# Kernel optimization log

Hardware: AMD Instinct MI355X
Metric: run time of the kernel (lower is better)

Reference implementation:

```python
import math
import jax, jax.numpy as jnp
import numpy as np
from jax import lax

# FPN anchor layout: 1024x768 image, strides {4,8,16,32,64}, 3 anchors/location
NUM_PER_LEVEL = (147456, 36864, 9216, 2304, 576)
A_TOTAL = sum(NUM_PER_LEVEL)
BATCH = 8
PRE_NMS_TOP_N = 1000   # testing
POST_NMS_TOP_N = 1000  # testing
NMS_THRESH = 0.7
SCORE_THRESH = 0.0
MIN_SIZE = 1.0
IMG_H, IMG_W = 768.0, 1024.0
BBOX_XFORM_CLIP = math.log(1000.0 / 16.0)


def setup_inputs() -> dict:
    key = jax.random.key(0)
    k1, k2, k3, k4, k5, k6 = jax.random.split(key, 6)
    objectness = jax.random.normal(k1, (BATCH, A_TOTAL), jnp.float32)
    pred_bbox_deltas = jax.random.normal(k2, (BATCH, A_TOTAL, 4), jnp.float32) * 0.2
    # valid anchor boxes (x1, y1, x2, y2)
    cx = jax.random.uniform(k3, (A_TOTAL,), jnp.float32) * IMG_W
    cy = jax.random.uniform(k4, (A_TOTAL,), jnp.float32) * IMG_H
    w = 16.0 + jax.random.uniform(k5, (A_TOTAL,), jnp.float32) * 176.0
    h = 16.0 + jax.random.uniform(k6, (A_TOTAL,), jnp.float32) * 176.0
    anchors = jnp.stack([cx - 0.5 * w, cy - 0.5 * h, cx + 0.5 * w, cy + 0.5 * h], -1)
    return {"objectness": objectness, "pred_bbox_deltas": pred_bbox_deltas, "anchors": anchors}


def _nms_image(boxes, scores, lvl, valid):
    """batched_nms (level-offset trick) + post-NMS top-k, fixed shapes.
    boxes [K,4], scores [K], lvl [K] int, valid [K] bool -> [POST_NMS_TOP_N, 5]"""
    K = boxes.shape[0]
    s = jnp.where(valid, scores, -1.0)
    order = jnp.argsort(-s)  # decreasing score (invalid last)
    b = boxes[order]
    s = s[order]
    v = valid[order]
    # offset boxes per level so cross-level boxes never overlap (torchvision batched_nms)
    offset = lvl[order].astype(b.dtype) * (jnp.max(lax.stop_gradient(boxes)) + 1.0)
    nb = lax.stop_gradient(b) + offset[:, None]
    area = (nb[:, 2] - nb[:, 0]) * (nb[:, 3] - nb[:, 1])
    lt = jnp.maximum(nb[:, None, :2], nb[None, :, :2])  # [K,K,2]
    rb = jnp.minimum(nb[:, None, 2:], nb[None, :, 2:])
    wh = jnp.clip(rb - lt, 0.0)
    inter = wh[..., 0] * wh[..., 1]
    iou = inter / jnp.maximum(area[:, None] + area[None, :] - inter, 1e-9)
    pos = jnp.arange(K)

    def body(keep, i):
        sup = keep[i] & (iou[i] > NMS_THRESH) & (pos > i)
        return keep & ~sup, None

    keep, _ = lax.scan(body, v, pos)
    masked = jnp.where(keep, s, -1.0)
    top_s, top_i = lax.top_k(masked, POST_NMS_TOP_N)  # kept, decreasing score
    sel_b = b[top_i]
    ok = top_s > -0.5
    sel_b = jnp.where(ok[:, None], sel_b, 0.0)
    top_s = jnp.where(ok, top_s, 0.0)
    return jnp.concatenate([sel_b, top_s[:, None]], axis=-1)


def reference(objectness, pred_bbox_deltas, anchors):
    # --- box decode (BoxCoder, weights (1,1,1,1)) ---
    wa = anchors[:, 2] - anchors[:, 0]
    ha = anchors[:, 3] - anchors[:, 1]
    cxa = anchors[:, 0] + 0.5 * wa
    cya = anchors[:, 1] + 0.5 * ha
    dx, dy = pred_bbox_deltas[..., 0], pred_bbox_deltas[..., 1]
    dw = jnp.minimum(pred_bbox_deltas[..., 2], BBOX_XFORM_CLIP)
    dh = jnp.minimum(pred_bbox_deltas[..., 3], BBOX_XFORM_CLIP)
    pcx = dx * wa + cxa
    pcy = dy * ha + cya
    pw = jnp.exp(dw) * wa
    ph = jnp.exp(dh) * ha
    proposals = jnp.stack(
        [pcx - 0.5 * pw, pcy - 0.5 * ph, pcx + 0.5 * pw, pcy + 0.5 * ph], axis=-1
    )  # [B, A, 4]

    # --- per-level pre-NMS top-k (_get_top_n_idx) ---
    levels = jnp.concatenate(
        [jnp.full((n,), i, jnp.int32) for i, n in enumerate(NUM_PER_LEVEL)]
    )
    idx_parts = []
    off = 0
    for n in NUM_PER_LEVEL:
        k = min(PRE_NMS_TOP_N, n)
        _, ti = lax.top_k(objectness[:, off:off + n], k)
        idx_parts.append(ti + off)
        off += n
    top_idx = jnp.concatenate(idx_parts, axis=1)  # [B, K]

    scores = jax.nn.sigmoid(jnp.take_along_axis(objectness, top_idx, axis=1))
    lvl = levels[top_idx]
    boxes = jnp.take_along_axis(proposals, top_idx[..., None], axis=1)  # [B,K,4]

    # --- clip to image ---
    x1 = jnp.clip(boxes[..., 0], 0.0, IMG_W)
    y1 = jnp.clip(boxes[..., 1], 0.0, IMG_H)
    x2 = jnp.clip(boxes[..., 2], 0.0, IMG_W)
    y2 = jnp.clip(boxes[..., 3], 0.0, IMG_H)
    boxes = jnp.stack([x1, y1, x2, y2], axis=-1)

    # remove_small_boxes + score threshold (as validity mask; fixed shapes)
    valid = ((x2 - x1) >= MIN_SIZE) & ((y2 - y1) >= MIN_SIZE) & (scores >= SCORE_THRESH)

    # --- per-image batched NMS + post-NMS top-k ---
    return jax.vmap(_nms_image)(boxes, scores, lvl, valid)  # [B, POST_NMS_TOP_N, 5]
```

## Files before the change

kernel.cpp:

```cpp
#include <hip/hip_runtime.h>
#include <math.h>

#pragma clang fp contract(off)

#define A_TOTAL 196416
#define BATCH 8
#define KTOT 4576
#define NLEV 5
#define MSPLIT 16
#define RCAP 6144

static __device__ const int d_aoff[NLEV] = {0, 147456, 184320, 193536, 195840};
static __device__ const int d_n[NLEV]    = {147456, 36864, 9216, 2304, 576};
static __device__ const int d_k[NLEV]    = {1000, 1000, 1000, 1000, 576};
static __device__ const int d_spl[NLEV]  = {8, 2, 1, 1, 1};
static __device__ const int d_bp[NLEV]   = {0, 8, 10, 11, 12};
static __device__ const int d_pb_l[13]    = {0,0,0,0,0,0,0,0,1,1,2,3,4};
static __device__ const int d_pb_part[13] = {0,1,2,3,4,5,6,7,0,1,0,0,0};

#define TM_IOU (0.699999988079071044921875 + 0x1p-25)

__device__ inline unsigned int mono(float f) {
  unsigned int u = __float_as_uint(f);
  return (u & 0x80000000u) ? ~u : (u | 0x80000000u);
}
__device__ inline float imono(unsigned int m) {
  return __uint_as_float((m & 0x80000000u) ? (m & 0x7FFFFFFFu) : ~m);
}

__device__ inline int cnt_gt(const float* A, int n, float s) {
  int lo = 0, hi = n;
  while (lo < hi) { int mid = (lo + hi) >> 1; if (A[mid] > s) lo = mid + 1; else hi = mid; }
  return lo;
}
__device__ inline int cnt_ge(const float* A, int n, float s) {
  int lo = 0, hi = n;
  while (lo < hi) { int mid = (lo + hi) >> 1; if (A[mid] >= s) lo = mid + 1; else hi = mid; }
  return lo;
}

__global__ __launch_bounds__(1024) void k_hist(const float* __restrict__ obj,
                                               int* __restrict__ hist_g,
                                               int* __restrict__ cnt_g,
                                               float* __restrict__ maxblk,
                                               float* __restrict__ out) {
  int blk = blockIdx.x;
  int tid = threadIdx.x;
  if (blk == 0) {
    for (int i = tid; i < 40; i += 1024) { maxblk[i] = 0.0f; cnt_g[i] = 0; }
  }
  int b = blk / 13, pb = blk % 13;
  if (pb == 0) {
    float* ob = out + (size_t)b * 5000;
    for (int i = tid; i < 5000; i += 1024) ob[i] = 0.0f;
  }
  int l = d_pb_l[pb], part = d_pb_part[pb];
  int slice = d_n[l] / d_spl[l];
  int start = d_aoff[l] + part * slice;
  const float4* p4 = (const float4*)(obj + (size_t)b * A_TOTAL + start);
  int s4 = slice >> 2;
  __shared__ int h[4096];
  for (int i = tid; i < 4096; i += 1024) h[i] = 0;
  __syncthreads();
  for (int i = tid; i < s4; i += 1024) {
    float4 v = p4[i];
    atomicAdd(&h[mono(v.x) >> 20], 1);
    atomicAdd(&h[mono(v.y) >> 20], 1);
    atomicAdd(&h[mono(v.z) >> 20], 1);
    atomicAdd(&h[mono(v.w) >> 20], 1);
  }
  __syncthreads();
  int* outp = hist_g + (size_t)blk * 4096;
  for (int i = tid; i < 4096; i += 1024) outp[i] = h[i];
}

__global__ __launch_bounds__(1024) void k_collect(const float* __restrict__ obj,
                                                  const int* __restrict__ hist_g,
                                                  int* __restrict__ cnt_g,
                                                  unsigned long long* __restrict__ cand_g) {
  int blk = blockIdx.x;
  int b = blk / 13, pb = blk % 13;
  int l = d_pb_l[pb], part = d_pb_part[pb];
  int bl = b * NLEV + l;
  const int k = d_k[l];
  int tid = threadIdx.x, lane = tid & 63;
  __shared__ int t[4096];
  __shared__ int grp[256];
  __shared__ unsigned int sP;
  __shared__ __align__(16) unsigned long long lbuf[RCAP];
  __shared__ int s_cnt, s_base;
  int parts = d_spl[l];
  const int* hb = hist_g + (size_t)(b * 13 + d_bp[l]) * 4096;
  for (int bin = tid; bin < 4096; bin += 1024) {
    int s = 0;
    for (int p = 0; p < parts; ++p) s += hb[p * 4096 + bin];
    t[bin] = s;
  }
  if (tid == 0) s_cnt = 0;
  __syncthreads();
  if (tid < 256) {
    int s = 0;
    for (int j = 0; j < 16; ++j) s += t[tid * 16 + j];
    grp[tid] = s;
  }
  __syncthreads();
  if (tid < 64) {
    int g0 = grp[4 * tid], g1 = grp[4 * tid + 1];
    int g2 = grp[4 * tid + 2], g3 = grp[4 * tid + 3];
    int q = g0 + g1 + g2 + g3;
    int x = q;
#pragma unroll
    for (int off = 1; off < 64; off <<= 1) {
      int y = __shfl_down(x, off);
      if (tid + off < 64) x += y;
    }
    int Qn = x - q;
    int best = -1;
    if (x >= k) best = 4 * tid;
    if (g1 + g2 + g3 + Qn >= k) best = 4 * tid + 1;
    if (g2 + g3 + Qn >= k) best = 4 * tid + 2;
    if (g3 + Qn >= k) best = 4 * tid + 3;
#pragma unroll
    for (int off = 1; off < 64; off <<= 1) best = max(best, __shfl_xor(best, off));
    int gstar = best;
    int partl = 0;
    if (4 * tid > gstar) partl += g0;
    if (4 * tid + 1 > gstar) partl += g1;
    if (4 * tid + 2 > gstar) partl += g2;
    if (4 * tid + 3 > gstar) partl += g3;
#pragma unroll
    for (int off = 1; off < 64; off <<= 1) partl += __shfl_xor(partl, off);
    int cum = partl;
    int tb = (tid < 16) ? t[gstar * 16 + tid] : 0;
    int Tx = tb;
#pragma unroll
    for (int off = 1; off < 16; off <<= 1) {
      int y = __shfl_down(Tx, off);
      if (tid + off < 16) Tx += y;
    }
    int bestd = -1;
    if (tid < 16 && cum + Tx >= k) bestd = tid;
#pragma unroll
    for (int off = 1; off < 64; off <<= 1) bestd = max(bestd, __shfl_xor(bestd, off));
    if (tid == 0) sP = (unsigned int)(gstar * 16 + bestd);
  }
  __syncthreads();
  unsigned int P = sP;
  int slice = d_n[l] / parts;
  int start = d_aoff[l] + part * slice;
  const float4* p4 = (const float4*)(obj + (size_t)b * A_TOTAL + start);
  int s4 = slice >> 2;
  int lbase = part * slice;
  for (int i = tid; i < s4; i += 1024) {
    float4 v = p4[i];
    unsigned int a[4] = {mono(v.x), mono(v.y), mono(v.z), mono(v.w)};
    bool q0 = (a[0] >> 20) >= P, q1 = (a[1] >> 20) >= P;
    bool q2 = (a[2] >> 20) >= P, q3 = (a[3] >> 20) >= P;
    if (__ballot(q0 | q1 | q2 | q3)) {
      bool qs[4] = {q0, q1, q2, q3};
#pragma unroll
      for (int c = 0; c < 4; ++c) {
        unsigned long long mb = __ballot(qs[c]);
        if (mb) {
          int base;
          if (lane == 0) base = atomicAdd(&s_cnt, __popcll(mb));
          base = __shfl(base, 0);
          if (qs[c]) {
            int slot = base + __popcll(mb & ((1ull << lane) - 1ull));
            if (slot < RCAP) {
              int idx = lbase + 4 * i + c;
              lbuf[slot] = ((unsigned long long)a[c] << 32) |
                           (unsigned int)(~(unsigned int)idx);
            }
          }
        }
      }
    }
  }
  __syncthreads();
  int cnt = min(s_cnt, RCAP);
  if (tid == 0) s_base = atomicAdd(&cnt_g[bl], cnt);
  __syncthreads();
  int base = s_base;
  for (int i = tid; i < cnt; i += 1024) {
    int slot = base + i;
    if (slot < RCAP) cand_g[(size_t)bl * RCAP + slot] = lbuf[i];
  }
}

__device__ inline float decode_emit(unsigned long long e, int rank, int b,
                                    int k, int aoff, int bl,
                                    const float* __restrict__ deltas,
                                    const float* __restrict__ anchors,
                                    float* __restrict__ sc0,
                                    float4* __restrict__ box0) {
  if (rank >= k) return 0.0f;
  unsigned int k32 = (unsigned int)(e >> 32);
  unsigned int idx = ~(unsigned int)(e & 0xFFFFFFFFull);
  float o = imono(k32);
  int gidx = aoff + (int)idx;
  const float* dl = deltas + ((size_t)b * A_TOTAL + gidx) * 4;
  const float* an = anchors + (size_t)gidx * 4;
  float a0 = an[0], a1 = an[1], a2 = an[2], a3 = an[3];
  float wa = a2 - a0, ha = a3 - a1;
  float cxa = a0 + 0.5f * wa, cya = a1 + 0.5f * ha;
  float dx = dl[0], dy = dl[1];
  const float CLIPV = 4.135166556742356f;
  float dw = fminf(dl[2], CLIPV), dh = fminf(dl[3], CLIPV);
  float pcx = dx * wa + cxa;
  float pcy = dy * ha + cya;
  float pw = (float)exp((double)dw) * wa;
  float ph = (float)exp((double)dh) * ha;
  float x1 = pcx - 0.5f * pw, y1 = pcy - 0.5f * ph;
  float x2 = pcx + 0.5f * pw, y2 = pcy + 0.5f * ph;
  x1 = fminf(fmaxf(x1, 0.0f), 1024.0f);
  x2 = fminf(fmaxf(x2, 0.0f), 1024.0f);
  y1 = fminf(fmaxf(y1, 0.0f), 768.0f);
  y2 = fminf(fmaxf(y2, 0.0f), 768.0f);
  float s = (float)(1.0 / (1.0 + exp(-(double)o)));
  bool valid = ((x2 - x1) >= 1.0f) && ((y2 - y1) >= 1.0f) && (s >= 0.0f);
  sc0[bl * 1024 + rank] = valid ? s : -1.0f;
  box0[bl * 1024 + rank] = make_float4(x1, y1, x2, y2);
  return fmaxf(fmaxf(x1, y1), fmaxf(x2, y2));
}

__global__ __launch_bounds__(1024) void k_rankdec(const unsigned long long* __restrict__ cand_g,
                                                  const int* __restrict__ cnt_g,
                                                  const float* __restrict__ deltas,
                                                  const float* __restrict__ anchors,
                                                  float* __restrict__ sc0,
                                                  float4* __restrict__ box0,
                                                  float* __restrict__ maxblk) {
  int bl = blockIdx.x;
  int b = bl / NLEV, l = bl % NLEV;
  const int k = d_k[l], aoff = d_aoff[l];
  int cnt = min(cnt_g[bl], RCAP);
  int tid = threadIdx.x, lane = tid & 63, w = tid >> 6;
  __shared__ int h[4096], sfx[4096], offs[4096];
  __shared__ __align__(16) unsigned long long sorted[RCAP];
  __shared__ int s_wsum[16];
  __shared__ unsigned int s_max;
  if (tid == 0) s_max = 0u;
  for (int i = tid; i < 4096; i += 1024) h[i] = 0;
  __syncthreads();
  const unsigned long long* src = cand_g + (size_t)bl * RCAP;
  for (int i = tid; i < cnt; i += 1024)
    atomicAdd(&h[(unsigned int)(src[i] >> 52)], 1);
  __syncthreads();
  int t4 = tid * 4;
  int h0 = h[t4], h1 = h[t4 + 1], h2 = h[t4 + 2], h3 = h[t4 + 3];
  int mysum = h0 + h1 + h2 + h3;
  int x = mysum;
#pragma unroll
  for (int off = 1; off < 64; off <<= 1) {
    int y = __shfl_down(x, off);
    if (lane + off < 64) x += y;
  }
  if (lane == 0) s_wsum[w] = x;
  __syncthreads();
  int wsuf = 0;
  for (int ww = w + 1; ww < 16; ++ww) wsuf += s_wsum[ww];
  int excl = (x - mysum) + wsuf;
  sfx[t4 + 3] = excl;
  sfx[t4 + 2] = excl + h3;
  sfx[t4 + 1] = excl + h3 + h2;
  sfx[t4]     = excl + h3 + h2 + h1;
  offs[t4] = sfx[t4]; offs[t4 + 1] = sfx[t4 + 1];
  offs[t4 + 2] = sfx[t4 + 2]; offs[t4 + 3] = sfx[t4 + 3];
  __syncthreads();
  for (int i = tid; i < cnt; i += 1024) {
    unsigned long long e = src[i];
    int pos = atomicAdd(&offs[(unsigned int)(e >> 52)], 1);
    sorted[pos] = e;
  }
  __syncthreads();
  float mx = 0.0f;
  for (int p = tid; p < cnt; p += 1024) {
    unsigned long long e = sorted[p];
    unsigned int bin = (unsigned int)(e >> 52);
    int s0 = sfx[bin], s1 = s0 + h[bin];
    int rank = s0;
    for (int j = s0; j < s1; ++j) rank += (sorted[j] > e);
    if (rank < k)
      mx = fmaxf(mx, decode_emit(e, rank, b, k, aoff, bl, deltas, anchors, sc0, box0));
  }
#pragma unroll
  for (int s = 1; s < 64; s <<= 1) mx = fmaxf(mx, __shfl_xor(mx, s));
  if (lane == 0) atomicMax(&s_max, __float_as_uint(mx));
  __syncthreads();
  if (tid == 0) maxblk[bl] = __uint_as_float(s_max);
}

__global__ __launch_bounds__(1024) void k_mask(const float* __restrict__ sc0,
                                               const float4* __restrict__ box0,
                                               const float* __restrict__ maxblk,
                                               float* __restrict__ lvlsc,
                                               float4* __restrict__ lvlraw,
                                               int* __restrict__ g_V,
                                               unsigned long long* __restrict__ masks) {
  int blk = blockIdx.x;
  int bl = blk / MSPLIT, part = blk % MSPLIT;
  int b = bl / NLEV, l = bl % NLEV;
  const int k = d_k[l];
  int tid = threadIdx.x, lane = tid & 63, w = tid >> 6;
  __shared__ float4 lbox[1024];
  __shared__ float s_mv;
  __shared__ int s_wcnt[16];
  if (w == 0) {
    float v = (lane < NLEV) ? maxblk[b * NLEV + lane] : 0.0f;
#pragma unroll
    for (int s = 1; s < 64; s <<= 1) v = fmaxf(v, __shfl_xor(v, s));
    if (lane == 0) s_mv = v;
  }
  bool in = tid < k;
  float s = in ? sc0[bl * 1024 + tid] : -1.0f;
  bool valid = in && (s >= 0.0f);
  unsigned long long mb = __ballot(valid);
  if (lane == 0) s_wcnt[w] = __popcll(mb);
  __syncthreads();
  int pre = 0;
  for (int ww = 0; ww < w; ++ww) pre += s_wcnt[ww];
  int j = pre + __popcll(mb & ((1ull << lane) - 1ull));
  int V = 0;
  for (int ww = 0; ww < 16; ++ww) V += s_wcnt[ww];
  float off = (float)l * (s_mv + 1.0f);
  if (valid) {
    float4 bx = box0[bl * 1024 + tid];
    lbox[j] = make_float4(bx.x + off, bx.y + off, bx.z + off, bx.w + off);
    if (part == 0) {
      lvlsc[bl * 1024 + j] = s;
      lvlraw[bl * 1024 + j] = bx;
    }
  }
  if (part == 0 && tid == 0) g_V[bl] = V;
  __syncthreads();
  int row0 = part * 64;
  if (row0 >= V) return;
  int i = row0 + lane;
  if (i >= V) return;
  float4 bb = lbox[i];
  float ba = (bb.z - bb.x) * (bb.w - bb.y);
  unsigned long long bits = 0ull;
  int jbase = w * 64;
  if (jbase + 63 > i && jbase < V) {
    int jhi = min(64, V - jbase);
    for (int jo = 0; jo < jhi; ++jo) {
      int jj = jbase + jo;
      float4 cb = lbox[jj];
      float ca = (cb.z - cb.x) * (cb.w - cb.y);
      float xx1 = fmaxf(bb.x, cb.x), yy1 = fmaxf(bb.y, cb.y);
      float xx2 = fminf(bb.z, cb.z), yy2 = fminf(bb.w, cb.w);
      float wd = fmaxf(xx2 - xx1, 0.0f), ht = fmaxf(yy2 - yy1, 0.0f);
      float inter = wd * ht;
      float denom = fmaxf(ba + ca - inter, 1e-9f);
      if ((jj > i) && ((double)inter >= TM_IOU * (double)denom)) bits |= (1ull << jo);
    }
  }
  masks[((size_t)bl * 16 + w) * 1024 + i] = bits;
}

__global__ __launch_bounds__(1024) void k_scan(const unsigned long long* __restrict__ masks,
                                               const int* __restrict__ g_V,
                                               const float* __restrict__ lvlsc,
                                               float* __restrict__ ksc_g,
                                               int* __restrict__ kj_g,
                                               int* __restrict__ K_g) {
  int bl = blockIdx.x;
  int tid = threadIdx.x, lane = tid & 63, w = tid >> 6;
  int V = g_V[bl];
  const int nch = (V + 63) / 64;
  const unsigned long long* M = masks + (size_t)bl * 16 * 1024;
  __shared__ unsigned long long s_remv[16];
  __shared__ unsigned long long s_D[2][72];
  __shared__ unsigned long long s_dw;
  __shared__ int s_wcnt[16];
  if (tid < 16) s_remv[tid] = ~0ull;
  int base_w = w * 64;
  unsigned long long init_w;
  if (V <= base_w) init_w = ~0ull;
  else if (V >= base_w + 64) init_w = 0ull;
  else init_w = (~0ull) << (V - base_w);
  if (w == 0 && nch > 0) s_D[0][lane] = (lane < V) ? M[lane] : 0ull;
  if (tid < 8) { s_D[0][64 + tid] = 0ull; s_D[1][64 + tid] = 0ull; }
  unsigned long long acc = 0ull;
  unsigned long long val_next = 0ull;
  if (w > 0 && w < nch && lane < V) val_next = M[(size_t)w * 1024 + lane];
  __syncthreads();

  for (int c = 0; c < nch; ++c) {
    unsigned long long val = val_next;
    val_next = 0ull;
    int rn = 64 * (c + 1) + lane;
    if (w > c + 1 && w < nch && rn < V) val_next = M[(size_t)w * 1024 + rn];
    if (w == c) {
      unsigned long long red = acc;
#pragma unroll
      for (int s = 1; s < 64; s <<= 1) red |= __shfl_xor(red, s);
      unsigned long long dw = init_w | red;
      const unsigned long long* D = s_D[c & 1];
      unsigned long long pb[8];
#pragma unroll
      for (int u = 0; u < 8; ++u) pb[u] = D[u];
#pragma unroll
      for (int g = 0; g < 8; ++g) {
#pragma unroll
        for (int u = 0; u < 8; ++u) {
          int jj = g * 8 + u;
          if (!((dw >> jj) & 1ull)) dw |= pb[u];
          pb[u] = D[jj + 8];
        }
      }
      if (lane == 0) { s_dw = dw; s_remv[c] = dw; }
    }
    if (w == c + 1 && w < nch) {
      int rr = 64 * (c + 1) + lane;
      s_D[(c + 1) & 1][lane] = (rr < V) ? M[(size_t)(c + 1) * 1024 + rr] : 0ull;
    }
    __syncthreads();
    if (w > c && w < nch) {
      unsigned long long kept = ~s_dw;
      if ((kept >> lane) & 1ull) acc |= val;
    }
    __syncthreads();
  }

  unsigned long long kb = ~s_remv[w];
  bool kept = ((kb >> lane) & 1ull) != 0ull;
  unsigned long long mb = __ballot(kept);
  if (lane == 0) s_wcnt[w] = __popcll(mb);
  __syncthreads();
  int pre = 0;
  for (int ww = 0; ww < w; ++ww) pre += s_wcnt[ww];
  int r = pre + __popcll(mb & ((1ull << lane) - 1ull));
  if (kept) {
    ksc_g[bl * 1024 + r] = lvlsc[bl * 1024 + tid];
    kj_g[bl * 1024 + r] = tid;
  }
  if (tid == 0) {
    int t = 0;
    for (int ww = 0; ww < 16; ++ww) t += s_wcnt[ww];
    K_g[bl] = t;
  }
}

__global__ __launch_bounds__(1024) void k_merge(const float* __restrict__ ksc_g,
                                                const int* __restrict__ kj_g,
                                                const int* __restrict__ K_g,
                                                const float4* __restrict__ lvlraw,
                                                float* __restrict__ out) {
  int blk = blockIdx.x;
  int b = blk / NLEV, l = blk % NLEV;
  int tid = threadIdx.x;
  __shared__ float ksc[NLEV * 1024];
  __shared__ int sK[NLEV];
  if (tid < NLEV) sK[tid] = K_g[b * NLEV + tid];
  __syncthreads();
  int K[NLEV];
  for (int l2 = 0; l2 < NLEV; ++l2) K[l2] = sK[l2];
  for (int l2 = 0; l2 < NLEV; ++l2) {
    for (int i = tid; i < K[l2]; i += 1024)
      ksc[l2 * 1024 + i] = ksc_g[(size_t)(b * NLEV + l2) * 1024 + i];
  }
  __syncthreads();
  if (tid < K[l]) {
    float s = ksc[l * 1024 + tid];
    int rank = tid;
    for (int l2 = 0; l2 < NLEV; ++l2) {
      if (l2 == l) continue;
      const float* A = ksc + l2 * 1024;
      rank += (l2 < l) ? cnt_ge(A, K[l2], s) : cnt_gt(A, K[l2], s);
    }
    if (rank < 1000) {
      int j = kj_g[(size_t)(b * NLEV + l) * 1024 + tid];
      float4 bx = lvlraw[(size_t)(b * NLEV + l) * 1024 + j];
      float* op = out + (size_t)b * 5000 + (size_t)rank * 5;
      op[0] = bx.x; op[1] = bx.y; op[2] = bx.z; op[3] = bx.w; op[4] = s;
    }
  }
}

extern "C" void kernel_launch(void* const* d_in, const int* in_sizes, int n_in,
                              void* d_out, int out_size, void* d_ws, size_t ws_size,
                              hipStream_t stream) {
  const float* obj     = (const float*)d_in[0];
  const float* deltas  = (const float*)d_in[1];
  const float* anchors = (const float*)d_in[2];
  float* out = (float*)d_out;

  char* p = (char*)d_ws;
  float4* box0   = (float4*)p; p += (size_t)40 * 1024 * sizeof(float4);
  float4* lvlraw = (float4*)p; p += (size_t)40 * 1024 * sizeof(float4);
  unsigned long long* cand_g = (unsigned long long*)p; p += (size_t)40 * RCAP * 8;
  unsigned long long* masks  = (unsigned long long*)p; p += (size_t)40 * 16 * 1024 * 8;
  int*   hist_g = (int*)p;   p += (size_t)104 * 4096 * 4;
  int*   cnt_g  = (int*)p;   p += 40 * 4;
  float* maxblk = (float*)p; p += 40 * 4;
  float* sc0    = (float*)p; p += (size_t)40 * 1024 * 4;
  float* lvlsc  = (float*)p; p += (size_t)40 * 1024 * 4;
  int*   g_V    = (int*)p;   p += 40 * 4;
  float* ksc_g  = (float*)p; p += (size_t)40 * 1024 * 4;
  int*   kj_g   = (int*)p;   p += (size_t)40 * 1024 * 4;
  int*   K_g    = (int*)p;   p += 40 * 4;

  hipLaunchKernelGGL(k_hist, dim3(BATCH * 13), dim3(1024), 0, stream,
                     obj, hist_g, cnt_g, maxblk, out);
  hipLaunchKernelGGL(k_collect, dim3(BATCH * 13), dim3(1024), 0, stream,
                     obj, hist_g, cnt_g, cand_g);
  hipLaunchKernelGGL(k_rankdec, dim3(BATCH * NLEV), dim3(1024), 0, stream,
                     cand_g, cnt_g, deltas, anchors, sc0, box0, maxblk);
  hipLaunchKernelGGL(k_mask, dim3(BATCH * NLEV * MSPLIT), dim3(1024), 0, stream,
                     sc0, box0, maxblk, lvlsc, lvlraw, g_V, masks);
  hipLaunchKernelGGL(k_scan, dim3(BATCH * NLEV), dim3(1024), 0, stream,
                     masks, g_V, lvlsc, ksc_g, kj_g, K_g);
  hipLaunchKernelGGL(k_merge, dim3(BATCH * NLEV), dim3(1024), 0, stream,
                     ksc_g, kj_g, K_g, lvlraw, out);
}
```

Baseline: 236.1 us.

## Split candidates into above-pivot and pivot-bin sets; rank by brute-force count across more blocks

k_collect now writes candidates strictly above the pivot bin and candidates inside the pivot bin into separate regions with separate counters. k_rankdec no longer does a per-level in-shared-memory bucket sort. It is split into 12 blocks of 256 threads per (image, level). Each thread ranks its two candidates by counting larger keys within its own group, above-pivot or pivot-bin. This spreads the ranking and decode work over 480 blocks instead of 40 to raise parallelism, at the cost of redundant candidate loads per block and quadratic comparisons. maxblk grows to one entry per part, and k_mask reduces across all of them.

```diff
diff --git a/kernel.cpp b/kernel.cpp
--- a/kernel.cpp
+++ b/kernel.cpp
@@ -9,6 +9,7 @@
 #define NLEV 5
 #define MSPLIT 16
 #define RCAP 6144
+#define NPARTS 12
 
 static __device__ const int d_aoff[NLEV] = {0, 147456, 184320, 193536, 195840};
 static __device__ const int d_n[NLEV]    = {147456, 36864, 9216, 2304, 576};
@@ -41,13 +42,15 @@
 
 __global__ __launch_bounds__(1024) void k_hist(const float* __restrict__ obj,
                                                int* __restrict__ hist_g,
-                                               int* __restrict__ cnt_g,
+                                               int* __restrict__ cnt_hi,
+                                               int* __restrict__ cnt_mid,
                                                float* __restrict__ maxblk,
                                                float* __restrict__ out) {
   int blk = blockIdx.x;
   int tid = threadIdx.x;
   if (blk == 0) {
-    for (int i = tid; i < 40; i += 1024) { maxblk[i] = 0.0f; cnt_g[i] = 0; }
+    for (int i = tid; i < 40 * NPARTS; i += 1024) maxblk[i] = 0.0f;
+    for (int i = tid; i < 40; i += 1024) { cnt_hi[i] = 0; cnt_mid[i] = 0; }
   }
   int b = blk / 13, pb = blk % 13;
   if (pb == 0) {
@@ -76,7 +79,8 @@
 
 __global__ __launch_bounds__(1024) void k_collect(const float* __restrict__ obj,
                                                   const int* __restrict__ hist_g,
-                                                  int* __restrict__ cnt_g,
+                                                  int* __restrict__ cnt_hi,
+                                                  int* __restrict__ cnt_mid,
                                                   unsigned long long* __restrict__ cand_g) {
   int blk = blockIdx.x;
   int b = blk / 13, pb = blk % 13;
@@ -88,7 +92,7 @@
   __shared__ int grp[256];
   __shared__ unsigned int sP;
   __shared__ __align__(16) unsigned long long lbuf[RCAP];
-  __shared__ int s_cnt, s_base;
+  __shared__ int s_hi, s_md, s_bh, s_bm;
   int parts = d_spl[l];
   const int* hb = hist_g + (size_t)(b * 13 + d_bp[l]) * 4096;
   for (int bin = tid; bin < 4096; bin += 1024) {
@@ -96,7 +100,7 @@
     for (int p = 0; p < parts; ++p) s += hb[p * 4096 + bin];
     t[bin] = s;
   }
-  if (tid == 0) s_cnt = 0;
+  if (tid == 0) { s_hi = 0; s_md = 0; }
   __syncthreads();
   if (tid < 256) {
     int s = 0;
@@ -154,37 +158,54 @@
   for (int i = tid; i < s4; i += 1024) {
     float4 v = p4[i];
     unsigned int a[4] = {mono(v.x), mono(v.y), mono(v.z), mono(v.w)};
-    bool q0 = (a[0] >> 20) >= P, q1 = (a[1] >> 20) >= P;
-    bool q2 = (a[2] >> 20) >= P, q3 = (a[3] >> 20) >= P;
-    if (__ballot(q0 | q1 | q2 | q3)) {
-      bool qs[4] = {q0, q1, q2, q3};
+    unsigned int bn[4] = {a[0] >> 20, a[1] >> 20, a[2] >> 20, a[3] >> 20};
+    bool any = (bn[0] >= P) | (bn[1] >= P) | (bn[2] >= P) | (bn[3] >= P);
+    if (__ballot(any)) {
 #pragma unroll
       for (int c = 0; c < 4; ++c) {
-        unsigned long long mb = __ballot(qs[c]);
-        if (mb) {
+        bool hi = bn[c] > P, md = bn[c] == P;
+        unsigned long long key = ((unsigned long long)a[c] << 32) |
+                                 (unsigned int)(~(unsigned int)(lbase + 4 * i + c));
+        unsigned long long mbh = __ballot(hi);
+        if (mbh) {
           int base;
-          if (lane == 0) base = atomicAdd(&s_cnt, __popcll(mb));
+          if (lane == 0) base = atomicAdd(&s_hi, __popcll(mbh));
           base = __shfl(base, 0);
-          if (qs[c]) {
-            int slot = base + __popcll(mb & ((1ull << lane) - 1ull));
-            if (slot < RCAP) {
-              int idx = lbase + 4 * i + c;
-              lbuf[slot] = ((unsigned long long)a[c] << 32) |
-                           (unsigned int)(~(unsigned int)idx);
-            }
+          if (hi) {
+            int slot = base + __popcll(mbh & ((1ull << lane) - 1ull));
+            if (slot < RCAP) lbuf[slot] = key;
+          }
+        }
+        unsigned long long mbm = __ballot(md);
+        if (mbm) {
+          int base;
+          if (lane == 0) base = atomicAdd(&s_md, __popcll(mbm));
+          base = __shfl(base, 0);
+          if (md) {
+            int m = base + __popcll(mbm & ((1ull << lane) - 1ull));
+            int slot = RCAP - 1 - m;
+            if (slot >= 0) lbuf[slot] = key;
           }
         }
       }
     }
   }
   __syncthreads();
-  int cnt = min(s_cnt, RCAP);
-  if (tid == 0) s_base = atomicAdd(&cnt_g[bl], cnt);
-  __syncthreads();
-  int base = s_base;
-  for (int i = tid; i < cnt; i += 1024) {
-    int slot = base + i;
+  int ch = min(s_hi, RCAP);
+  int cm = min(s_md, RCAP - ch);
+  if (tid == 0) {
+    s_bh = atomicAdd(&cnt_hi[bl], ch);
+    s_bm = atomicAdd(&cnt_mid[bl], cm);
+  }
+  __syncthreads();
+  int bh = s_bh, bm = s_bm;
+  for (int i = tid; i < ch; i += 1024) {
+    int slot = bh + i;
     if (slot < RCAP) cand_g[(size_t)bl * RCAP + slot] = lbuf[i];
+  }
+  for (int i = tid; i < cm; i += 1024) {
+    int gpos = RCAP - bm - cm + i;
+    if (gpos >= 0) cand_g[(size_t)bl * RCAP + gpos] = lbuf[RCAP - cm + i];
   }
 }
 
@@ -224,71 +245,68 @@
   return fmaxf(fmaxf(x1, y1), fmaxf(x2, y2));
 }
 
-__global__ __launch_bounds__(1024) void k_rankdec(const unsigned long long* __restrict__ cand_g,
-                                                  const int* __restrict__ cnt_g,
-                                                  const float* __restrict__ deltas,
-                                                  const float* __restrict__ anchors,
-                                                  float* __restrict__ sc0,
-                                                  float4* __restrict__ box0,
-                                                  float* __restrict__ maxblk) {
-  int bl = blockIdx.x;
+__global__ __launch_bounds__(256) void k_rankdec(const unsigned long long* __restrict__ cand_g,
+                                                 const int* __restrict__ cnt_hi,
+                                                 const int* __restrict__ cnt_mid,
+                                                 const float* __restrict__ deltas,
+                                                 const float* __restrict__ anchors,
+                                                 float* __restrict__ sc0,
+                                                 float4* __restrict__ box0,
+                                                 float* __restrict__ maxblk) {
+  int bl = blockIdx.x / NPARTS, part = blockIdx.x % NPARTS;
   int b = bl / NLEV, l = bl % NLEV;
   const int k = d_k[l], aoff = d_aoff[l];
-  int cnt = min(cnt_g[bl], RCAP);
-  int tid = threadIdx.x, lane = tid & 63, w = tid >> 6;
-  __shared__ int h[4096], sfx[4096], offs[4096];
-  __shared__ __align__(16) unsigned long long sorted[RCAP];
-  __shared__ int s_wsum[16];
+  int A = min(cnt_hi[bl], RCAP);
+  int M = min(cnt_mid[bl], RCAP - A);
+  int A2 = (A + 1) & ~1, M2 = (M + 1) & ~1;
+  int T = A2 + M2;
+  if (part * 512 >= T) return;
+  __shared__ __align__(16) unsigned long long cb[RCAP + 2];
   __shared__ unsigned int s_max;
+  int tid = threadIdx.x;
   if (tid == 0) s_max = 0u;
-  for (int i = tid; i < 4096; i += 1024) h[i] = 0;
-  __syncthreads();
   const unsigned long long* src = cand_g + (size_t)bl * RCAP;
-  for (int i = tid; i < cnt; i += 1024)
-    atomicAdd(&h[(unsigned int)(src[i] >> 52)], 1);
-  __syncthreads();
-  int t4 = tid * 4;
-  int h0 = h[t4], h1 = h[t4 + 1], h2 = h[t4 + 2], h3 = h[t4 + 3];
-  int mysum = h0 + h1 + h2 + h3;
-  int x = mysum;
-#pragma unroll
-  for (int off = 1; off < 64; off <<= 1) {
-    int y = __shfl_down(x, off);
-    if (lane + off < 64) x += y;
-  }
-  if (lane == 0) s_wsum[w] = x;
-  __syncthreads();
-  int wsuf = 0;
-  for (int ww = w + 1; ww < 16; ++ww) wsuf += s_wsum[ww];
-  int excl = (x - mysum) + wsuf;
-  sfx[t4 + 3] = excl;
-  sfx[t4 + 2] = excl + h3;
-  sfx[t4 + 1] = excl + h3 + h2;
-  sfx[t4]     = excl + h3 + h2 + h1;
-  offs[t4] = sfx[t4]; offs[t4 + 1] = sfx[t4 + 1];
-  offs[t4 + 2] = sfx[t4 + 2]; offs[t4 + 3] = sfx[t4 + 3];
-  __syncthreads();
-  for (int i = tid; i < cnt; i += 1024) {
-    unsigned long long e = src[i];
-    int pos = atomicAdd(&offs[(unsigned int)(e >> 52)], 1);
-    sorted[pos] = e;
-  }
-  __syncthreads();
+  for (int i = tid; i < A; i += 256) cb[i] = src[i];
+  for (int i = tid; i < M; i += 256) cb[A2 + i] = src[RCAP - M + i];
+  if (tid == 0) {
+    if (A & 1) cb[A] = 0ull;
+    if (M & 1) cb[A2 + M] = 0ull;
+  }
+  __syncthreads();
+  int p0 = part * 512 + tid, p1 = p0 + 256;
+  unsigned long long e0 = (p0 < T) ? cb[p0] : 0ull;
+  unsigned long long e1 = (p1 < T) ? cb[p1] : 0ull;
+  int lo0, n0, ba0, lo1, n1, ba1;
+  if (p0 < A2) { lo0 = 0; n0 = A2 >> 1; ba0 = 0; }
+  else         { lo0 = A2 >> 1; n0 = M2 >> 1; ba0 = A; }
+  if (p1 < A2) { lo1 = 0; n1 = A2 >> 1; ba1 = 0; }
+  else         { lo1 = A2 >> 1; n1 = M2 >> 1; ba1 = A; }
+  int r0 = 0, r1 = 0;
+  const ulonglong2* c2 = (const ulonglong2*)cb;
+  if (lo0 == lo1) {
+    for (int j = lo0; j < lo0 + n0; ++j) {
+      ulonglong2 v = c2[j];
+      r0 += (v.x > e0) + (v.y > e0);
+      r1 += (v.x > e1) + (v.y > e1);
+    }
+  } else {
+    for (int j = lo0; j < lo0 + n0; ++j) {
+      ulonglong2 v = c2[j];
+      r0 += (v.x > e0) + (v.y > e0);
+    }
+    for (int j = lo1; j < lo1 + n1; ++j) {
+      ulonglong2 v = c2[j];
+      r1 += (v.x > e1) + (v.y > e1);
+    }
+  }
   float mx = 0.0f;
-  for (int p = tid; p < cnt; p += 1024) {
-    unsigned long long e = sorted[p];
-    unsigned int bin = (unsigned int)(e >> 52);
-    int s0 = sfx[bin], s1 = s0 + h[bin];
-    int rank = s0;
-    for (int j = s0; j < s1; ++j) rank += (sorted[j] > e);
-    if (rank < k)
-      mx = fmaxf(mx, decode_emit(e, rank, b, k, aoff, bl, deltas, anchors, sc0, box0));
-  }
+  if (e0) mx = fmaxf(mx, decode_emit(e0, ba0 + r0, b, k, aoff, bl, deltas, anchors, sc0, box0));
+  if (e1) mx = fmaxf(mx, decode_emit(e1, ba1 + r1, b, k, aoff, bl, deltas, anchors, sc0, box0));
 #pragma unroll
   for (int s = 1; s < 64; s <<= 1) mx = fmaxf(mx, __shfl_xor(mx, s));
-  if (lane == 0) atomicMax(&s_max, __float_as_uint(mx));
-  __syncthreads();
-  if (tid == 0) maxblk[bl] = __uint_as_float(s_max);
+  if ((tid & 63) == 0) atomicMax(&s_max, __float_as_uint(mx));
+  __syncthreads();
+  if (tid == 0) maxblk[blockIdx.x] = __uint_as_float(s_max);
 }
 
 __global__ __launch_bounds__(1024) void k_mask(const float* __restrict__ sc0,
@@ -307,7 +325,9 @@
   __shared__ float s_mv;
   __shared__ int s_wcnt[16];
   if (w == 0) {
-    float v = (lane < NLEV) ? maxblk[b * NLEV + lane] : 0.0f;
+    float v = 0.0f;
+    for (int i = lane; i < NLEV * NPARTS; i += 64)
+      v = fmaxf(v, maxblk[b * (NLEV * NPARTS) + i]);
 #pragma unroll
     for (int s = 1; s < 64; s <<= 1) v = fmaxf(v, __shfl_xor(v, s));
     if (lane == 0) s_mv = v;
@@ -493,8 +513,9 @@
   unsigned long long* cand_g = (unsigned long long*)p; p += (size_t)40 * RCAP * 8;
   unsigned long long* masks  = (unsigned long long*)p; p += (size_t)40 * 16 * 1024 * 8;
   int*   hist_g = (int*)p;   p += (size_t)104 * 4096 * 4;
-  int*   cnt_g  = (int*)p;   p += 40 * 4;
-  float* maxblk = (float*)p; p += 40 * 4;
+  int*   cnt_hi = (int*)p;   p += 40 * 4;
+  int*   cnt_mid= (int*)p;   p += 40 * 4;
+  float* maxblk = (float*)p; p += (size_t)40 * NPARTS * 4;
   float* sc0    = (float*)p; p += (size_t)40 * 1024 * 4;
   float* lvlsc  = (float*)p; p += (size_t)40 * 1024 * 4;
   int*   g_V    = (int*)p;   p += 40 * 4;
@@ -503,11 +524,11 @@
   int*   K_g    = (int*)p;   p += 40 * 4;
 
   hipLaunchKernelGGL(k_hist, dim3(BATCH * 13), dim3(1024), 0, stream,
-                     obj, hist_g, cnt_g, maxblk, out);
+                     obj, hist_g, cnt_hi, cnt_mid, maxblk, out);
   hipLaunchKernelGGL(k_collect, dim3(BATCH * 13), dim3(1024), 0, stream,
-                     obj, hist_g, cnt_g, cand_g);
-  hipLaunchKernelGGL(k_rankdec, dim3(BATCH * NLEV), dim3(1024), 0, stream,
-                     cand_g, cnt_g, deltas, anchors, sc0, box0, maxblk);
+                     obj, hist_g, cnt_hi, cnt_mid, cand_g);
+  hipLaunchKernelGGL(k_rankdec, dim3(BATCH * NLEV * NPARTS), dim3(256), 0, stream,
+                     cand_g, cnt_hi, cnt_mid, deltas, anchors, sc0, box0, maxblk);
   hipLaunchKernelGGL(k_mask, dim3(BATCH * NLEV * MSPLIT), dim3(1024), 0, stream,
                      sc0, box0, maxblk, lvlsc, lvlraw, g_V, masks);
   hipLaunchKernelGGL(k_scan, dim3(BATCH * NLEV), dim3(1024), 0, stream,
```

Result: slower. 251.8 us (+6.6%).
